# Optimization experiments

Measured on AMD Instinct MI355X. Metric: run time of the kernel, lower is better.

Reference implementation:

```python
import jax, jax.numpy as jnp
import numpy as np
import math


def cos_map(N):
    # DCT-II basis: weight[n, x] = cos(n*pi*(x+0.5)/N) * sqrt(2/N), row 0 scaled by 1/sqrt(2)
    wx = (jnp.arange(N, dtype=jnp.float32) + 0.5) / N
    wn = jnp.arange(N, dtype=jnp.float32)[:, None]
    w = jnp.cos(wn * wx[None, :] * jnp.pi) * math.sqrt(2.0 / N)
    return w.at[0, :].multiply(1.0 / math.sqrt(2.0))


def decay_map(H, W):
    wn = jnp.linspace(0.0, jnp.pi, H + 1)[:H][:, None]
    wm = jnp.linspace(0.0, jnp.pi, W + 1)[:W][None, :]
    return jnp.exp(-(wn ** 2 + wm ** 2))  # [H, W]


def layer_norm(x, g, b, eps=1e-5):
    mu = jnp.mean(x, axis=-1, keepdims=True)
    var = jnp.mean(jnp.square(x - mu), axis=-1, keepdims=True)
    return (x - mu) * jax.lax.rsqrt(var + eps) * g + b


def depthwise_conv3x3(x, w, b):
    # x: [B,C,H,W], w: [C,1,3,3] (groups=C), padding=1
    out = jax.lax.conv_general_dilated(
        x, w, window_strides=(1, 1), padding=((1, 1), (1, 1)),
        dimension_numbers=('NCHW', 'OIHW', 'NCHW'), feature_group_count=x.shape[1])
    return out + b[None, :, None, None]


def setup_inputs() -> dict:
    key = jax.random.key(0)
    ks = jax.random.split(key, 10)
    B, C, H, W = 16, 384, 64, 64
    x = jax.random.normal(ks[0], (B, C, H, W), jnp.float32)
    freq_embed = jax.random.normal(ks[1], (B, H, W, C), jnp.float32)
    dw_w = jax.random.normal(ks[2], (C, 1, 3, 3), jnp.float32) * 0.1
    dw_b = jax.random.normal(ks[3], (C,), jnp.float32) * 0.02
    lin_w = jax.random.normal(ks[4], (2 * C, C), jnp.float32) * 0.02
    lin_b = jnp.zeros((2 * C,), jnp.float32)
    tok_w = jax.random.normal(ks[5], (C, C), jnp.float32) * 0.02
    tok_b = jnp.zeros((C,), jnp.float32)
    ln_g = jnp.ones((C,), jnp.float32)
    ln_b = jnp.zeros((C,), jnp.float32)
    out_w = jax.random.normal(ks[6], (C, C), jnp.float32) * 0.02
    out_b = jnp.zeros((C,), jnp.float32)
    c = jnp.ones((1,), jnp.float32)
    alpha = jnp.ones((1,), jnp.float32) * 0.1
    return dict(x=x, freq_embed=freq_embed, dw_w=dw_w, dw_b=dw_b, lin_w=lin_w,
                lin_b=lin_b, tok_w=tok_w, tok_b=tok_b, ln_g=ln_g, ln_b=ln_b,
                out_w=out_w, out_b=out_b, c=c, alpha=alpha)


def reference(x, freq_embed, dw_w, dw_b, lin_w, lin_b, tok_w, tok_b,
              ln_g, ln_b, out_w, out_b, c, alpha):
    B, C, H, W = x.shape
    eps = 1e-8
    xd = depthwise_conv3x3(x, dw_w, dw_b)                       # [B,C,H,W]
    xcl = jnp.transpose(xd, (0, 2, 3, 1))                       # [B,H,W,C]
    xz = xcl @ lin_w.T + lin_b                                  # [B,H,W,2C]
    xs, z = jnp.split(xz, 2, axis=-1)
    Wn = cos_map(H)                                             # [H,H] (freq n, space h)
    Wm = cos_map(W)                                             # [W,W]
    # DCT2D: A(n,m) = sum_{h,w} Wn[n,h] Wm[m,w] phi(h,w)
    Xf = jnp.einsum('nh,bhwc->bnwc', Wn, xs)
    Xf = jnp.einsum('mw,bnwc->bnmc', Wm, Xf)                    # [B,H,W,C] freq domain
    x_u0 = Xf
    x_v0 = Xf  # original computes DCT2D(x) twice (identical)
    # learned time / decay modulation
    t = jax.nn.gelu(freq_embed @ tok_w.T + tok_b, approximate=False)  # [B,H,W,C]
    c_t = c * t
    cos_term = jnp.cos(c_t)
    sin_term = jnp.sin(c_t) / (c + eps)
    final = cos_term * x_u0 + sin_term * (x_v0 + (alpha / 2.0) * x_u0)
    wexp = decay_map(H, W)                                      # [H,W]
    final = final * jnp.power(wexp[None, :, :, None], t)        # freq-dependent decay e^{-(n^2+m^2)t}
    # IDCT2D: u(h,w) = sum_{n,m} Wn[n,h] Wm[m,w] A(n,m)
    xo = jnp.einsum('nh,bnmc->bhmc', Wn, final)
    xo = jnp.einsum('mw,bhmc->bhwc', Wm, xo)                    # [B,H,W,C]
    xo = layer_norm(xo, ln_g, ln_b)
    xo = xo * jax.nn.silu(z)
    out = xo @ out_w.T + out_b                                  # [B,H,W,C]
    return out
```

## Files before the change

### kernel.cpp

```cpp
#include <hip/hip_runtime.h>
#include <hip/hip_bf16.h>
#include <math.h>


typedef __attribute__((ext_vector_type(8))) short short8;
typedef __attribute__((ext_vector_type(4))) float floatx4;

#define PIF 3.14159265358979323846f

__device__ __forceinline__ short f2bf(float f) {
    union { float f; unsigned u; } v; v.f = f;
    unsigned r = v.u + 0x7fffu + ((v.u >> 16) & 1u);
    return (short)(r >> 16);
}
__device__ __forceinline__ float bf2f(short s) {
    union { unsigned u; float f; } v;
    v.u = ((unsigned)(unsigned short)s) << 16;
    return v.f;
}
__device__ __forceinline__ float fast_erf(float x) {
    float ax = fabsf(x);
    float t = 1.0f / fmaf(0.3275911f, ax, 1.0f);
    float poly = t * fmaf(t, fmaf(t, fmaf(t, fmaf(t, 1.061405429f, -1.453152027f),
                                          1.421413741f), -0.284496736f), 0.254829592f);
    float er = 1.0f - poly * __expf(-ax * ax);
    return copysignf(er, x);
}

__device__ __forceinline__ void gload16(const short* g, short* l) {
    __builtin_amdgcn_global_load_lds(
        (const __attribute__((address_space(1))) void*)g,
        (__attribute__((address_space(3))) void*)l, 16, 0, 0);
}

__device__ __forceinline__ int swi(int r, int c) {
    return (r << 6) + (c ^ ((((r) & 7) ^ ((r >> 3) & 7)) << 3));
}

__global__ __launch_bounds__(256) void k_f2bf(const float* __restrict__ src,
                                              short* __restrict__ dst, int n) {
    int i = (blockIdx.x * 256 + threadIdx.x) * 4;
    if (i < n) {
        float4 f = *(const float4*)(src + i);
        short4 o;
        o.x = f2bf(f.x); o.y = f2bf(f.y); o.z = f2bf(f.z); o.w = f2bf(f.w);
        *(short4*)(dst + i) = o;
    }
}

__global__ __launch_bounds__(256) void k_build_dct(short* __restrict__ wn,
                                                   short* __restrict__ wnt) {
    int i = blockIdx.x * 256 + threadIdx.x;
    if (i < 4096) {
        int n = i >> 6, h = i & 63;
        float v = cosf((float)n * ((float)h + 0.5f) * (PIF / 64.0f)) * sqrtf(2.0f / 64.0f);
        if (n == 0) v *= 0.70710678118654752f;
        short b = f2bf(v);
        wn[n * 64 + h]  = b;
        wnt[h * 64 + n] = b;
    }
}

__global__ __launch_bounds__(256) void k_conv(const float* __restrict__ x,
                                              const float* __restrict__ w,
                                              const float* __restrict__ bias,
                                              short* __restrict__ out) {
    __shared__ float sp[4096];
    int bc = blockIdx.x;
    int c = bc % 384;
    int tid = threadIdx.x;
    const float* xp = x + (size_t)bc * 4096;
    for (int i = 0; i < 4; i++) {
        int e = i * 1024 + tid * 4;
        *(float4*)(sp + e) = *(const float4*)(xp + e);
    }
    float wt[9];
    #pragma unroll
    for (int j = 0; j < 9; j++) wt[j] = w[c * 9 + j];
    float bv = bias[c];
    __syncthreads();
    short* op = out + (size_t)bc * 4096;
    for (int i = 0; i < 16; i++) {
        int hw = i * 256 + tid;
        int h = hw >> 6, ww = hw & 63;
        float acc = bv;
        #pragma unroll
        for (int dh = 0; dh < 3; dh++) {
            int ih = h + dh - 1;
            if (ih < 0 || ih > 63) continue;
            #pragma unroll
            for (int dw = 0; dw < 3; dw++) {
                int iw = ww + dw - 1;
                if (iw < 0 || iw > 63) continue;
                acc += sp[ih * 64 + iw] * wt[dh * 3 + dw];
            }
        }
        op[hw] = f2bf(acc);
    }
}

__global__ __launch_bounds__(256) void k_pl2tok(const short* __restrict__ src,
                                                short* __restrict__ dst) {
    __shared__ short tile[64 * 66];
    int ct = blockIdx.x, ht = blockIdx.y, b = blockIdx.z;
    int tid = threadIdx.x;
    const short* sp = src + ((size_t)b * 384 + ct * 64) * 4096 + ht * 64;
    for (int i = 0; i < 16; i++) {
        int idx = i * 256 + tid;
        int r = idx >> 6, col = idx & 63;
        tile[r * 66 + col] = sp[(size_t)r * 4096 + col];
    }
    __syncthreads();
    short* dp = dst + ((size_t)b * 4096 + ht * 64) * 384 + ct * 64;
    for (int i = 0; i < 16; i++) {
        int idx = i * 256 + tid;
        int r = idx >> 6, col = idx & 63;
        dp[(size_t)r * 384 + col] = tile[col * 66 + r];
    }
}

__device__ __forceinline__ void mm_core(const short* __restrict__ A,
                                        const short* __restrict__ Bw,
                                        int row_base, int col_base,
                                        short* smem, floatx4 (&acc)[4][4]) {
    const int K = 384;
    int tid = threadIdx.x;
    int wid = tid >> 6, lane = tid & 63;
    int quad = lane >> 4, l16 = lane & 15;
    int rowh = (wid >> 1) * 64, colh = (wid & 1) * 64;
    short* ldsA = smem;
    short* ldsB = smem + 8192;
    const short* ga = A + (size_t)row_base * K;
    const short* gb = Bw + (size_t)col_base * K;

    int q0 = tid, q1 = 256 + tid;
    int r0 = q0 >> 2, o0 = ((q0 & 3) ^ ((q0 >> 3) & 3)) * 8;
    int r1 = q1 >> 2, o1 = ((q1 & 3) ^ ((q1 >> 3) & 3)) * 8;
    short* la0 = ldsA + (wid * 64) * 8;
    short* la1 = ldsA + (256 + wid * 64) * 8;
    short* lb0 = ldsB + (wid * 64) * 8;
    short* lb1 = ldsB + (256 + wid * 64) * 8;

    auto stage = [&](int ks, int buf) {
        int k0 = ks * 32;
        gload16(ga + (size_t)r0 * K + k0 + o0, la0 + buf * 4096);
        gload16(ga + (size_t)r1 * K + k0 + o1, la1 + buf * 4096);
        gload16(gb + (size_t)r0 * K + k0 + o0, lb0 + buf * 4096);
        gload16(gb + (size_t)r1 * K + k0 + o1, lb1 + buf * 4096);
    };

    int ksw = (quad ^ ((l16 >> 1) & 3)) * 8;

    stage(0, 0);
    __syncthreads();
    #pragma unroll 2
    for (int ks = 0; ks < 12; ++ks) {
        int cur = ks & 1;
        if (ks < 11) stage(ks + 1, cur ^ 1);
        short8 af[4], bfr[4];
        #pragma unroll
        for (int s = 0; s < 4; s++) {
            af[s]  = *(const short8*)(ldsA + cur * 4096 + (rowh + s * 16 + l16) * 32 + ksw);
            bfr[s] = *(const short8*)(ldsB + cur * 4096 + (colh + s * 16 + l16) * 32 + ksw);
        }
        #pragma unroll
        for (int i = 0; i < 4; i++)
            #pragma unroll
            for (int j = 0; j < 4; j++)
                acc[i][j] = __builtin_amdgcn_mfma_f32_16x16x32_bf16(af[i], bfr[j], acc[i][j], 0, 0, 0);
        __syncthreads();
    }
}

__global__ __launch_bounds__(256) void k_gemm_split(const short* __restrict__ A,
                                                    const short* __restrict__ Bw,
                                                    const float* __restrict__ bias,
                                                    short* __restrict__ xs_pl,
                                                    short* __restrict__ z_tok) {
    __shared__ __align__(16) short smem[17408];
    int bid = blockIdx.x;
    int xcd = bid & 7, local = bid >> 3;
    int bx = local % 6;
    int by = xcd * 64 + local / 6;
    int row_base = by * 128, col_base = bx * 128;
    int tid = threadIdx.x;
    int wid = tid >> 6, lane = tid & 63, quad = lane >> 4, l16 = lane & 15;
    int rowh = (wid >> 1) * 64, colh = (wid & 1) * 64;

    floatx4 zero = {0.f, 0.f, 0.f, 0.f};
    floatx4 acc[4][4];
    #pragma unroll
    for (int i = 0; i < 4; i++)
        #pragma unroll
        for (int j = 0; j < 4; j++) acc[i][j] = zero;

    mm_core(A, Bw, row_base, col_base, smem, acc);

    if (bx < 3) {
        #pragma unroll
        for (int i = 0; i < 4; i++)
            #pragma unroll
            for (int j = 0; j < 4; j++) {
                int cl = colh + j * 16 + l16;
                float bs = bias[col_base + cl];
                #pragma unroll
                for (int r = 0; r < 4; r++) {
                    int rl = rowh + i * 16 + quad * 4 + r;
                    smem[cl * 136 + rl] = f2bf(acc[i][j][r] + bs);
                }
            }
        __syncthreads();
        int t0 = row_base;
        int b = t0 >> 12, hw0 = t0 & 4095;
        for (int it = 0; it < 8; it++) {
            int q = it * 256 + tid;
            int cl = q >> 4, t8 = (q & 15) * 8;
            short8 vv = *(const short8*)(smem + cl * 136 + t8);
            int c = col_base + cl;
            *(short8*)(xs_pl + ((size_t)b * 384 + c) * 4096 + hw0 + t8) = vv;
        }
    } else {
        #pragma unroll
        for (int i = 0; i < 4; i++)
            #pragma unroll
            for (int j = 0; j < 4; j++) {
                int col = col_base + colh + j * 16 + l16;
                float bs = bias[col];
                int cc = col - 384;
                #pragma unroll
                for (int r = 0; r < 4; r++) {
                    int row = row_base + rowh + i * 16 + quad * 4 + r;
                    z_tok[(size_t)row * 384 + cc] = f2bf(acc[i][j][r] + bs);
                }
            }
    }
}

__global__ __launch_bounds__(256) void k_gemm_mod(const short* __restrict__ A,
                                                  const short* __restrict__ Bw,
                                                  const float* __restrict__ bias,
                                                  short* __restrict__ Dpl) {
    __shared__ __align__(16) short smem[17408];
    int bid = blockIdx.x;
    int xcd = bid & 7, local = bid >> 3;
    int bx = local % 3;
    int by = xcd * 64 + local / 3;
    int row_base = by * 128, col_base = bx * 128;
    int tid = threadIdx.x;
    int wid = tid >> 6, lane = tid & 63, quad = lane >> 4, l16 = lane & 15;
    int rowh = (wid >> 1) * 64, colh = (wid & 1) * 64;

    floatx4 zero = {0.f, 0.f, 0.f, 0.f};
    floatx4 acc[4][4];
    #pragma unroll
    for (int i = 0; i < 4; i++)
        #pragma unroll
        for (int j = 0; j < 4; j++) acc[i][j] = zero;

    mm_core(A, Bw, row_base, col_base, smem, acc);

    #pragma unroll
    for (int i = 0; i < 4; i++) {
        #pragma unroll
        for (int j = 0; j < 4; j++) {
            int cl = colh + j * 16 + l16;
            float bs = bias[col_base + cl];
            #pragma unroll
            for (int r = 0; r < 4; r++) {
                int rl = rowh + i * 16 + quad * 4 + r;
                smem[cl * 136 + rl] = f2bf(acc[i][j][r] + bs);
            }
        }
    }
    __syncthreads();
    int t0 = row_base;
    int b = t0 >> 12, hw0 = t0 & 4095;
    for (int it = 0; it < 8; it++) {
        int q = it * 256 + tid;
        int cl = q >> 4, t8 = (q & 15) * 8;
        short8 vv = *(const short8*)(smem + cl * 136 + t8);
        int c = col_base + cl;
        *(short8*)(Dpl + ((size_t)b * 384 + c) * 4096 + hw0 + t8) = vv;
    }
}

__global__ __launch_bounds__(256) void k_spectral(const short* __restrict__ xs,
                                                  const short* __restrict__ vpl,
                                                  const short* __restrict__ wn,
                                                  const short* __restrict__ wnt,
                                                  const float* __restrict__ cp,
                                                  const float* __restrict__ ap,
                                                  short* __restrict__ xo) {
    __shared__ short sWn[4096], sWt[4096], sP[4096], sM[4096], sT[4096];
    int bc = blockIdx.x;
    int tid = threadIdx.x;
    int wid = tid >> 6, lane = tid & 63, quad = lane >> 4, l16 = lane & 15;
    const short* xp = xs + (size_t)bc * 4096;
    const short* mp = vpl + (size_t)bc * 4096;
    floatx4 zero = {0.f, 0.f, 0.f, 0.f};

    for (int i = 0; i < 2; i++) {
        int e = i * 2048 + tid * 8;
        int row = e >> 6, slot = (e >> 3) & 7;
        int gx = (row << 6) + (((slot ^ (row & 7) ^ ((row >> 3) & 7)) & 7) << 3);
        *(short8*)(sWn + e) = *(const short8*)(wn + gx);
        *(short8*)(sWt + e) = *(const short8*)(wnt + gx);
        *(short8*)(sM + e)  = *(const short8*)(mp + gx);
        short8 pv = *(const short8*)(xp + e);
        int h = row, w0 = e & 63;
        #pragma unroll
        for (int j = 0; j < 8; j++) sP[swi(w0 + j, h)] = pv[j];
    }
    __syncthreads();

    int mrow = wid * 16;
    floatx4 acc[4];

    #pragma unroll
    for (int j = 0; j < 4; j++) acc[j] = zero;
    #pragma unroll
    for (int ks = 0; ks < 2; ks++) {
        int k0 = ks * 32 + quad * 8;
        short8 a = *(const short8*)(sWn + swi(mrow + l16, k0));
        #pragma unroll
        for (int j = 0; j < 4; j++) {
            short8 b = *(const short8*)(sP + swi(j * 16 + l16, k0));
            acc[j] = __builtin_amdgcn_mfma_f32_16x16x32_bf16(a, b, acc[j], 0, 0, 0);
        }
    }
    #pragma unroll
    for (int j = 0; j < 4; j++)
        #pragma unroll
        for (int r = 0; r < 4; r++)
            sT[swi(mrow + quad * 4 + r, j * 16 + l16)] = f2bf(acc[j][r]);
    __syncthreads();

    #pragma unroll
    for (int j = 0; j < 4; j++) acc[j] = zero;
    #pragma unroll
    for (int ks = 0; ks < 2; ks++) {
        int k0 = ks * 32 + quad * 8;
        short8 a = *(const short8*)(sT + swi(mrow + l16, k0));
        #pragma unroll
        for (int j = 0; j < 4; j++) {
            short8 b = *(const short8*)(sWn + swi(j * 16 + l16, k0));
            acc[j] = __builtin_amdgcn_mfma_f32_16x16x32_bf16(a, b, acc[j], 0, 0, 0);
        }
    }
    __syncthreads();
    {
        float cv = cp[0], av = ap[0];
        float inv_c = 1.0f / (cv + 1e-8f);
        float gfac = 1.0f + 0.5f * av;
        #pragma unroll
        for (int j = 0; j < 4; j++)
            #pragma unroll
            for (int r = 0; r < 4; r++) {
                int n = mrow + quad * 4 + r, m = j * 16 + l16;
                float v = bf2f(sM[swi(n, m)]);
                float t = 0.5f * v * (1.0f + fast_erf(v * 0.70710678118654752f));
                float sn, cs;
                __sincosf(cv * t, &sn, &cs);
                float fac = cs + sn * inv_c * gfac;
                float wnf = (float)n * (PIF / 64.0f);
                float wmf = (float)m * (PIF / 64.0f);
                float mod = fac * __expf(-(wnf * wnf + wmf * wmf) * t);
                sP[swi(m, n)] = f2bf(acc[j][r] * mod);
            }
    }
    __syncthreads();

    #pragma unroll
    for (int j = 0; j < 4; j++) acc[j] = zero;
    #pragma unroll
    for (int ks = 0; ks < 2; ks++) {
        int k0 = ks * 32 + quad * 8;
        short8 a = *(const short8*)(sWt + swi(mrow + l16, k0));
        #pragma unroll
        for (int j = 0; j < 4; j++) {
            short8 b = *(const short8*)(sP + swi(j * 16 + l16, k0));
            acc[j] = __builtin_amdgcn_mfma_f32_16x16x32_bf16(a, b, acc[j], 0, 0, 0);
        }
    }
    __syncthreads();
    #pragma unroll
    for (int j = 0; j < 4; j++)
        #pragma unroll
        for (int r = 0; r < 4; r++)
            sT[swi(mrow + quad * 4 + r, j * 16 + l16)] = f2bf(acc[j][r]);
    __syncthreads();

    #pragma unroll
    for (int j = 0; j < 4; j++) acc[j] = zero;
    #pragma unroll
    for (int ks = 0; ks < 2; ks++) {
        int k0 = ks * 32 + quad * 8;
        short8 a = *(const short8*)(sT + swi(mrow + l16, k0));
        #pragma unroll
        for (int j = 0; j < 4; j++) {
            short8 b = *(const short8*)(sWt + swi(j * 16 + l16, k0));
            acc[j] = __builtin_amdgcn_mfma_f32_16x16x32_bf16(a, b, acc[j], 0, 0, 0);
        }
    }
    short* op = xo + (size_t)bc * 4096;
    #pragma unroll
    for (int j = 0; j < 4; j++)
        #pragma unroll
        for (int r = 0; r < 4; r++) {
            int h = mrow + quad * 4 + r, w = j * 16 + l16;
            op[h * 64 + w] = f2bf(acc[j][r]);
        }
}

__global__ __launch_bounds__(256) void k_lnfuse(const short* __restrict__ xo_pl,
                                                const short* __restrict__ z,
                                                const float* __restrict__ g,
                                                const float* __restrict__ bb,
                                                short* __restrict__ y) {
    __shared__ short tile[32 * 392];
    __shared__ float smu[32], srstd[32];
    int tid = threadIdx.x;
    int t0 = blockIdx.x * 32;
    int b = t0 >> 12, hw0 = t0 & 4095;

    for (int it = 0; it < 6; it++) {
        int m = it * 256 + tid;
        int c = m >> 2, t8 = (m & 3) * 8;
        short8 v = *(const short8*)(xo_pl + ((size_t)b * 384 + c) * 4096 + hw0 + t8);
        #pragma unroll
        for (int j = 0; j < 8; j++) tile[(t8 + j) * 392 + c] = v[j];
    }
    __syncthreads();

    {
        int t = tid >> 3, g8 = tid & 7;
        const short* trow = tile + t * 392 + g8 * 48;
        float s = 0.f, sq = 0.f;
        #pragma unroll
        for (int i = 0; i < 6; i++) {
            short8 xv = *(const short8*)(trow + i * 8);
            #pragma unroll
            for (int j = 0; j < 8; j++) {
                float f = bf2f(xv[j]);
                s += f; sq += f * f;
            }
        }
        s  += __shfl_xor(s, 1, 64);  s  += __shfl_xor(s, 2, 64);  s  += __shfl_xor(s, 4, 64);
        sq += __shfl_xor(sq, 1, 64); sq += __shfl_xor(sq, 2, 64); sq += __shfl_xor(sq, 4, 64);
        if (g8 == 0) {
            float mu = s * (1.0f / 384.0f);
            float var = sq * (1.0f / 384.0f) - mu * mu;
            smu[t] = mu;
            srstd[t] = rsqrtf(var + 1e-5f);
        }
    }
    __syncthreads();

    for (int it = 0; it < 6; it++) {
        int m = it * 256 + tid;
        int tok = m / 48, ch = (m - tok * 48) * 8;
        float mu = smu[tok], rstd = srstd[tok];
        short8 xv = *(const short8*)(tile + tok * 392 + ch);
        const size_t goff = (size_t)(t0 + tok) * 384 + ch;
        short8 zv = *(const short8*)(z + goff);
        float4 g0 = *(const float4*)(g + ch);
        float4 g1 = *(const float4*)(g + ch + 4);
        float4 b0 = *(const float4*)(bb + ch);
        float4 b1 = *(const float4*)(bb + ch + 4);
        float gv[8] = {g0.x, g0.y, g0.z, g0.w, g1.x, g1.y, g1.z, g1.w};
        float bv[8] = {b0.x, b0.y, b0.z, b0.w, b1.x, b1.y, b1.z, b1.w};
        short8 ov;
        #pragma unroll
        for (int j = 0; j < 8; j++) {
            float zz = bf2f(zv[j]);
            float sil = zz / (1.f + __expf(-zz));
            float o = (bf2f(xv[j]) - mu) * rstd * gv[j] + bv[j];
            ov[j] = f2bf(o * sil);
        }
        *(short8*)(y + goff) = ov;
    }
}

__global__ __launch_bounds__(256) void k_gemm_f32out(const short* __restrict__ A,
                                                     const short* __restrict__ Bw,
                                                     const float* __restrict__ bias,
                                                     float* __restrict__ D) {
    __shared__ __align__(16) short smem[17408];
    const int N = 384;
    int bid = blockIdx.x;
    int xcd = bid & 7, local = bid >> 3;
    int bx = local % 3;
    int by = xcd * 64 + local / 3;
    int row_base = by * 128, col_base = bx * 128;
    int tid = threadIdx.x;
    int wid = tid >> 6, lane = tid & 63, quad = lane >> 4, l16 = lane & 15;
    int rowh = (wid >> 1) * 64, colh = (wid & 1) * 64;

    floatx4 zero = {0.f, 0.f, 0.f, 0.f};
    floatx4 acc[4][4];
    #pragma unroll
    for (int i = 0; i < 4; i++)
        #pragma unroll
        for (int j = 0; j < 4; j++) acc[i][j] = zero;

    mm_core(A, Bw, row_base, col_base, smem, acc);

    #pragma unroll
    for (int i = 0; i < 4; i++) {
        #pragma unroll
        for (int j = 0; j < 4; j++) {
            int col = col_base + colh + j * 16 + l16;
            float bs = bias[col];
            #pragma unroll
            for (int r = 0; r < 4; r++) {
                int row = row_base + rowh + i * 16 + quad * 4 + r;
                D[(size_t)row * N + col] = acc[i][j][r] + bs;
            }
        }
    }
}

extern "C" void kernel_launch(void* const* d_in, const int* in_sizes, int n_in,
                              void* d_out, int out_size, void* d_ws, size_t ws_size,
                              hipStream_t stream) {
    const float* x     = (const float*)d_in[0];
    const float* freq  = (const float*)d_in[1];
    const float* dw_w  = (const float*)d_in[2];
    const float* dw_b  = (const float*)d_in[3];
    const float* lin_w = (const float*)d_in[4];
    const float* lin_b = (const float*)d_in[5];
    const float* tok_w = (const float*)d_in[6];
    const float* tok_b = (const float*)d_in[7];
    const float* ln_g  = (const float*)d_in[8];
    const float* ln_b  = (const float*)d_in[9];
    const float* out_w = (const float*)d_in[10];
    const float* out_b = (const float*)d_in[11];
    const float* cp    = (const float*)d_in[12];
    const float* ap    = (const float*)d_in[13];
    float* out = (float*)d_out;
    (void)in_sizes; (void)n_in; (void)ws_size;

    const size_t TC = (size_t)65536 * 384;
    short* bufA = (short*)d_out;
    short* bufB = (short*)d_out + TC;

    char* ws = (char*)d_ws;
    size_t off = 0;
    auto alloc = [&](size_t bytes) {
        char* p = ws + off; off += (bytes + 255) & ~(size_t)255; return p;
    };
    short* wn_bf   = (short*)alloc(4096 * 2);
    short* wnt_bf  = (short*)alloc(4096 * 2);
    short* linw_bf = (short*)alloc((size_t)294912 * 2);
    short* tokw_bf = (short*)alloc((size_t)147456 * 2);
    short* outw_bf = (short*)alloc((size_t)147456 * 2);
    short* bufC    = (short*)alloc(TC * 2);
    short* bufE    = (short*)alloc(TC * 2);

    k_f2bf<<<288, 256, 0, stream>>>(lin_w, linw_bf, 294912);
    k_f2bf<<<144, 256, 0, stream>>>(tok_w, tokw_bf, 147456);
    k_f2bf<<<144, 256, 0, stream>>>(out_w, outw_bf, 147456);
    k_build_dct<<<16, 256, 0, stream>>>(wn_bf, wnt_bf);

    k_conv<<<6144, 256, 0, stream>>>(x, dw_w, dw_b, bufE);
    k_pl2tok<<<dim3(6, 64, 16), 256, 0, stream>>>(bufE, bufC);
    k_gemm_split<<<3072, 256, 0, stream>>>(bufC, linw_bf, lin_b,
                                           bufA, bufB);
    k_f2bf<<<24576, 256, 0, stream>>>(freq, bufE, 25165824);
    k_gemm_mod<<<1536, 256, 0, stream>>>(bufE, tokw_bf, tok_b,
                                         bufC);
    k_spectral<<<6144, 256, 0, stream>>>(bufA, bufC, wn_bf, wnt_bf,
                                         cp, ap, bufE);
    k_lnfuse<<<2048, 256, 0, stream>>>(bufE, bufB, ln_g, ln_b, bufC);
    k_gemm_f32out<<<1536, 256, 0, stream>>>(bufC, outw_bf, out_b, out);
}
```

Measured before the change: 502.2 us.

## Merge prep kernels, vectorize transpose and bf16 cast, add occupancy hints

The four small weight-cast and DCT-basis kernels become a single launch. The plane-to-token transpose now uses 16-byte global loads and stores through an XOR-swizzled shared tile instead of scalar 2-byte accesses. The large freq_embed cast handles 8 elements per thread, and the three GEMMs get a minimum-occupancy hint of 3 blocks. Together these aim to cut launch overhead and memory-transaction count, though the occupancy hint may force register spills in the GEMMs.

```diff
diff --git a/kernel.cpp b/kernel.cpp
--- a/kernel.cpp
+++ b/kernel.cpp
@@ -37,28 +37,45 @@
     return (r << 6) + (c ^ ((((r) & 7) ^ ((r >> 3) & 7)) << 3));
 }
 
-__global__ __launch_bounds__(256) void k_f2bf(const float* __restrict__ src,
-                                              short* __restrict__ dst, int n) {
-    int i = (blockIdx.x * 256 + threadIdx.x) * 4;
-    if (i < n) {
+__global__ __launch_bounds__(256) void k_prep(const float* __restrict__ lin_w,
+                                              const float* __restrict__ tok_w,
+                                              const float* __restrict__ out_w,
+                                              short* __restrict__ linw_bf,
+                                              short* __restrict__ tokw_bf,
+                                              short* __restrict__ outw_bf,
+                                              short* __restrict__ wn,
+                                              short* __restrict__ wnt) {
+    int b = blockIdx.x;
+    if (b < 576) {
+        const float* src; short* dst; int base;
+        if (b < 288)      { src = lin_w; dst = linw_bf; base = b; }
+        else if (b < 432) { src = tok_w; dst = tokw_bf; base = b - 288; }
+        else              { src = out_w; dst = outw_bf; base = b - 432; }
+        int i = (base * 256 + threadIdx.x) * 4;
         float4 f = *(const float4*)(src + i);
         short4 o;
         o.x = f2bf(f.x); o.y = f2bf(f.y); o.z = f2bf(f.z); o.w = f2bf(f.w);
         *(short4*)(dst + i) = o;
-    }
-}
-
-__global__ __launch_bounds__(256) void k_build_dct(short* __restrict__ wn,
-                                                   short* __restrict__ wnt) {
-    int i = blockIdx.x * 256 + threadIdx.x;
-    if (i < 4096) {
+    } else {
+        int i = (b - 576) * 256 + threadIdx.x;
         int n = i >> 6, h = i & 63;
         float v = cosf((float)n * ((float)h + 0.5f) * (PIF / 64.0f)) * sqrtf(2.0f / 64.0f);
         if (n == 0) v *= 0.70710678118654752f;
-        short b = f2bf(v);
-        wn[n * 64 + h]  = b;
-        wnt[h * 64 + n] = b;
-    }
+        short bb = f2bf(v);
+        wn[n * 64 + h]  = bb;
+        wnt[h * 64 + n] = bb;
+    }
+}
+
+__global__ __launch_bounds__(256) void k_f2bf8(const float* __restrict__ src,
+                                               short* __restrict__ dst) {
+    int i = (blockIdx.x * 256 + threadIdx.x) * 8;
+    float4 a = *(const float4*)(src + i);
+    float4 b = *(const float4*)(src + i + 4);
+    short8 o;
+    o[0] = f2bf(a.x); o[1] = f2bf(a.y); o[2] = f2bf(a.z); o[3] = f2bf(a.w);
+    o[4] = f2bf(b.x); o[5] = f2bf(b.y); o[6] = f2bf(b.z); o[7] = f2bf(b.w);
+    *(short8*)(dst + i) = o;
 }
 
 __global__ __launch_bounds__(256) void k_conv(const float* __restrict__ x,
@@ -101,21 +118,26 @@
 
 __global__ __launch_bounds__(256) void k_pl2tok(const short* __restrict__ src,
                                                 short* __restrict__ dst) {
-    __shared__ short tile[64 * 66];
+    __shared__ short tile[4096];
     int ct = blockIdx.x, ht = blockIdx.y, b = blockIdx.z;
     int tid = threadIdx.x;
     const short* sp = src + ((size_t)b * 384 + ct * 64) * 4096 + ht * 64;
-    for (int i = 0; i < 16; i++) {
-        int idx = i * 256 + tid;
-        int r = idx >> 6, col = idx & 63;
-        tile[r * 66 + col] = sp[(size_t)r * 4096 + col];
+    #pragma unroll
+    for (int i = 0; i < 2; i++) {
+        int q = i * 256 + tid;
+        int r = q >> 3, c8 = (q & 7) * 8;
+        short8 v = *(const short8*)(sp + (size_t)r * 4096 + c8);
+        #pragma unroll
+        for (int j = 0; j < 8; j++) tile[swi(c8 + j, r)] = v[j];
     }
     __syncthreads();
     short* dp = dst + ((size_t)b * 4096 + ht * 64) * 384 + ct * 64;
-    for (int i = 0; i < 16; i++) {
-        int idx = i * 256 + tid;
-        int r = idx >> 6, col = idx & 63;
-        dp[(size_t)r * 384 + col] = tile[col * 66 + r];
+    #pragma unroll
+    for (int i = 0; i < 2; i++) {
+        int q = i * 256 + tid;
+        int r2 = q >> 3, c8 = (q & 7) * 8;
+        short8 v = *(const short8*)(tile + swi(r2, c8));
+        *(short8*)(dp + (size_t)r2 * 384 + c8) = v;
     }
 }
 
@@ -172,11 +194,11 @@
     }
 }
 
-__global__ __launch_bounds__(256) void k_gemm_split(const short* __restrict__ A,
-                                                    const short* __restrict__ Bw,
-                                                    const float* __restrict__ bias,
-                                                    short* __restrict__ xs_pl,
-                                                    short* __restrict__ z_tok) {
+__global__ __launch_bounds__(256, 3) void k_gemm_split(const short* __restrict__ A,
+                                                       const short* __restrict__ Bw,
+                                                       const float* __restrict__ bias,
+                                                       short* __restrict__ xs_pl,
+                                                       short* __restrict__ z_tok) {
     __shared__ __align__(16) short smem[17408];
     int bid = blockIdx.x;
     int xcd = bid & 7, local = bid >> 3;
@@ -236,10 +258,10 @@
     }
 }
 
-__global__ __launch_bounds__(256) void k_gemm_mod(const short* __restrict__ A,
-                                                  const short* __restrict__ Bw,
-                                                  const float* __restrict__ bias,
-                                                  short* __restrict__ Dpl) {
+__global__ __launch_bounds__(256, 3) void k_gemm_mod(const short* __restrict__ A,
+                                                     const short* __restrict__ Bw,
+                                                     const float* __restrict__ bias,
+                                                     short* __restrict__ Dpl) {
     __shared__ __align__(16) short smem[17408];
     int bid = blockIdx.x;
     int xcd = bid & 7, local = bid >> 3;
@@ -481,10 +503,10 @@
     }
 }
 
-__global__ __launch_bounds__(256) void k_gemm_f32out(const short* __restrict__ A,
-                                                     const short* __restrict__ Bw,
-                                                     const float* __restrict__ bias,
-                                                     float* __restrict__ D) {
+__global__ __launch_bounds__(256, 3) void k_gemm_f32out(const short* __restrict__ A,
+                                                        const short* __restrict__ Bw,
+                                                        const float* __restrict__ bias,
+                                                        float* __restrict__ D) {
     __shared__ __align__(16) short smem[17408];
     const int N = 384;
     int bid = blockIdx.x;
@@ -557,16 +579,14 @@
     short* bufC    = (short*)alloc(TC * 2);
     short* bufE    = (short*)alloc(TC * 2);
 
-    k_f2bf<<<288, 256, 0, stream>>>(lin_w, linw_bf, 294912);
-    k_f2bf<<<144, 256, 0, stream>>>(tok_w, tokw_bf, 147456);
-    k_f2bf<<<144, 256, 0, stream>>>(out_w, outw_bf, 147456);
-    k_build_dct<<<16, 256, 0, stream>>>(wn_bf, wnt_bf);
+    k_prep<<<592, 256, 0, stream>>>(lin_w, tok_w, out_w,
+                                    linw_bf, tokw_bf, outw_bf, wn_bf, wnt_bf);
 
     k_conv<<<6144, 256, 0, stream>>>(x, dw_w, dw_b, bufE);
     k_pl2tok<<<dim3(6, 64, 16), 256, 0, stream>>>(bufE, bufC);
     k_gemm_split<<<3072, 256, 0, stream>>>(bufC, linw_bf, lin_b,
                                            bufA, bufB);
-    k_f2bf<<<24576, 256, 0, stream>>>(freq, bufE, 25165824);
+    k_f2bf8<<<12288, 256, 0, stream>>>(freq, bufE);
     k_gemm_mod<<<1536, 256, 0, stream>>>(bufE, tokw_bf, tok_b,
                                          bufC);
     k_spectral<<<6144, 256, 0, stream>>>(bufA, bufC, wn_bf, wnt_bf,
```

Measured after the change: 479.1 us. 4.6% less time.
